# Kernel optimization log

Hardware: AMD Instinct MI355X
Metric: run time of the kernel (lower is better)

Reference implementation:

```python
import jax, jax.numpy as jnp
import numpy as np

N, IN_DIM, HID, OUT_DIM = 1024, 128, 128, 128


def setup_inputs() -> dict:
    key = jax.random.key(0)
    ks = jax.random.split(key, 7)
    s_in = 1.0 / np.sqrt(IN_DIM)
    s_h = 1.0 / np.sqrt(HID)
    return {
        "x": jax.random.normal(ks[0], (N, IN_DIM), jnp.float32),
        "W1": jax.random.normal(ks[1], (IN_DIM, HID), jnp.float32) * s_in,
        "b1": jax.random.normal(ks[2], (HID,), jnp.float32) * s_in,
        "W2": jax.random.normal(ks[3], (HID, 1), jnp.float32) * s_h,
        "b2": jax.random.normal(ks[4], (1,), jnp.float32) * s_h,
        "Wg": jax.random.normal(ks[5], (IN_DIM, OUT_DIM), jnp.float32) * s_in,
        "bg": jax.random.normal(ks[6], (OUT_DIM,), jnp.float32) * s_in,
    }


def reference(x, W1, b1, W2, b2, Wg, bg):
    # Pairwise abs-diff: [N, N, in_dim]
    diff = jnp.abs(x[:, None, :] - x[None, :, :])
    # 2-layer MLP -> scalar edge logit, then sigmoid -> dense adjacency [N, N]
    h = jax.nn.relu(jnp.einsum("ijd,dh->ijh", diff, W1) + b1)
    adj = jax.nn.sigmoid(jnp.einsum("ijh,ho->ijo", h, W2)[..., 0] + b2[0])
    # sigmoid > 0 everywhere => dense_to_sparse keeps ALL N^2 edges incl. diagonal;
    # PyG gcn_norm then adds no extra self-loops. Symmetric GCN normalization:
    deg = adj.sum(axis=1)  # adj is symmetric (|x_i - x_j| symmetric)
    dinv = jax.lax.rsqrt(deg)
    a_norm = dinv[:, None] * adj * dinv[None, :]
    out = a_norm @ (x @ Wg) + bg
    out = jnp.where(out > 0, out, 0.2 * out)  # leaky_relu(0.2)
    return out, adj
```

## Files before the change

kernel.cpp:

```cpp
#include <hip/hip_runtime.h>
#include <hip/hip_bf16.h>
#include <math.h>

typedef __attribute__((ext_vector_type(8))) _Float16 half8;
typedef __attribute__((ext_vector_type(2))) _Float16 half2v;
typedef __attribute__((ext_vector_type(4))) float f32x4;
typedef __attribute__((ext_vector_type(4))) unsigned int u32x4;

#define NPT 1024
#define D   128

__device__ __forceinline__ unsigned int absdiff_pk(unsigned int a, unsigned int b) {
  half2v d = __builtin_bit_cast(half2v, a) - __builtin_bit_cast(half2v, b);
  return __builtin_bit_cast(unsigned int, d) & 0x7FFF7FFFu;
}
__device__ __forceinline__ unsigned int pk_max(unsigned int a, unsigned int b) {
  unsigned int r;
  asm("v_pk_max_f16 %0, %1, %2" : "=v"(r) : "v"(a), "v"(b));
  return r;
}
__device__ __forceinline__ unsigned int pkrtz(float lo, float hi) {
  return __builtin_bit_cast(unsigned int, __builtin_amdgcn_cvt_pkrtz(lo, hi));
}
__device__ __forceinline__ float fdot2(unsigned int a, unsigned int b, float c) {
  return __builtin_amdgcn_fdot2(__builtin_bit_cast(half2v, a),
                                __builtin_bit_cast(half2v, b), c, false);
}

__global__ __launch_bounds__(128) void k_prep(const float* __restrict__ x,
                                              const float* __restrict__ W1,
                                              const float* __restrict__ Wg,
                                              unsigned short* __restrict__ xsw,
                                              unsigned short* __restrict__ w1p,
                                              unsigned short* __restrict__ xwghT) {
  __shared__ float xi[D];
  const int i = blockIdx.x;
  const int t = threadIdx.x;
  const float xv = x[i * D + t];
  xi[t] = xv;
  const _Float16 hv = (_Float16)xv;
  const int byte = i * 256 + ((2 * t) ^ ((i & 7) << 4));
  *(unsigned short*)((unsigned char*)xsw + byte) =
      __builtin_bit_cast(unsigned short, hv);
  if (i < 128) {
    const _Float16 wv = (_Float16)W1[t * 128 + i];
    w1p[((t >> 3) * 128 + i) * 8 + (t & 7)] = __builtin_bit_cast(unsigned short, wv);
  }
  __syncthreads();
  float a0 = 0.f, a1 = 0.f, a2 = 0.f, a3 = 0.f;
#pragma unroll 8
  for (int k = 0; k < D; k += 4) {
    a0 += xi[k + 0] * Wg[(k + 0) * D + t];
    a1 += xi[k + 1] * Wg[(k + 1) * D + t];
    a2 += xi[k + 2] * Wg[(k + 2) * D + t];
    a3 += xi[k + 3] * Wg[(k + 3) * D + t];
  }
  const _Float16 av = (_Float16)((a0 + a1) + (a2 + a3));
  xwghT[t * NPT + i] = __builtin_bit_cast(unsigned short, av);
}

__global__ __launch_bounds__(256, 2) void k_adj(const unsigned short* __restrict__ xsw,
                                                const unsigned short* __restrict__ w1p,
                                                const float* __restrict__ b1,
                                                const float* __restrict__ W2,
                                                const float* __restrict__ b2,
                                                float* __restrict__ adj) {
  __shared__ float sbuf[4][272];
  const int tid  = threadIdx.x;
  const int lane = tid & 63;
  const int w    = tid >> 6;
  const int l15  = lane & 15;
  const int g    = lane >> 4;
  const int i   = blockIdx.x * 4 + w;
  const int c   = blockIdx.y;
  const int i2  = 1023 - i;
  const int a   = i >> 4;
  const int n_i = 64 - a;
  const int ustart = c * 16;
  const int uend   = (c == 3) ? 65 : (ustart + 16);
  const int len    = uend - ustart;
  const int nvals  = len * 16;
  const int asc    = (blockIdx.x & 1) == 0;

  half8 w1f[4][8];
#pragma unroll
  for (int ks = 0; ks < 4; ++ks)
#pragma unroll
    for (int ht = 0; ht < 8; ++ht)
      w1f[ks][ht] = *(const half8*)(w1p + ((ks * 4 + g) * 128 + ht * 16 + l15) * 8);

  unsigned int nb1pk[8][2], w2pk[8][2];
  float c0 = 0.f;
#pragma unroll
  for (int ht = 0; ht < 8; ++ht) {
    const f32x4 bv = *(const f32x4*)&b1[ht * 16 + g * 4];
    const f32x4 wv = *(const f32x4*)&W2[ht * 16 + g * 4];
    c0 += bv[0] * wv[0] + bv[1] * wv[1] + bv[2] * wv[2] + bv[3] * wv[3];
    nb1pk[ht][0] = pkrtz(-bv[0], -bv[1]);
    nb1pk[ht][1] = pkrtz(-bv[2], -bv[3]);
    w2pk[ht][0] = pkrtz(wv[0], wv[1]);
    w2pk[ht][1] = pkrtz(wv[2], wv[3]);
  }
  c0 += __shfl_xor(c0, 16);
  c0 += __shfl_xor(c0, 32);
  const float B2 = b2[0] + c0;

  const unsigned char* xsb = (const unsigned char*)xsw;
  const unsigned char* jlane = xsb + l15 * 256;
  const int sxJ = (l15 & 7) << 4;
  const int kb0 = (0 * 64 + g * 16) ^ sxJ;
  const int kb1 = (1 * 64 + g * 16) ^ sxJ;
  const int kb2 = (2 * 64 + g * 16) ^ sxJ;
  const int kb3 = (3 * 64 + g * 16) ^ sxJ;

  float* sbw = sbuf[w];
  u32x4 xiu[4];
  int row_cur = -1;

  u32x4 jr0, jr1, jr2, jr3;
  {
    const int u0 = asc ? ustart : (uend - 1);
    const int grp0 = (u0 < n_i) ? (a + u0) : (u0 - 1);
    const unsigned char* cur = jlane + grp0 * 4096;
    jr0 = *(const u32x4*)(cur + kb0);
    jr1 = *(const u32x4*)(cur + kb1);
    jr2 = *(const u32x4*)(cur + kb2);
    jr3 = *(const u32x4*)(cur + kb3);
  }

#pragma unroll 1
  for (int t = 0; t < len; ++t) {
    const int u = asc ? (ustart + t) : (uend - 1 - t);
    const int row = (u < n_i) ? i : i2;
    if (row != row_cur) {
      row_cur = row;
      const unsigned char* xrow = xsb + row * 256;
      const int sxI = (row & 7) << 4;
#pragma unroll
      for (int ks = 0; ks < 4; ++ks)
        xiu[ks] = *(const u32x4*)(xrow + ((ks * 64 + g * 16) ^ sxI));
    }
    const int tn = (t + 1 < len) ? (t + 1) : t;
    const int un = asc ? (ustart + tn) : (uend - 1 - tn);
    const int grpn = (un < n_i) ? (a + un) : (un - 1);
    const unsigned char* nrow = jlane + grpn * 4096;

    f32x4 acc[8];
#pragma unroll
    for (int ht = 0; ht < 8; ++ht) acc[ht] = f32x4{0.f, 0.f, 0.f, 0.f};

    __builtin_amdgcn_s_setprio(1);
    {
      u32x4 afu;
#pragma unroll
      for (int p4 = 0; p4 < 4; ++p4) afu[p4] = absdiff_pk(jr0[p4], xiu[0][p4]);
      jr0 = *(const u32x4*)(nrow + kb0);
      const half8 af = __builtin_bit_cast(half8, afu);
#pragma unroll
      for (int ht = 0; ht < 8; ++ht)
        acc[ht] = __builtin_amdgcn_mfma_f32_16x16x32_f16(w1f[0][ht], af, acc[ht], 0, 0, 0);
    }
    {
      u32x4 afu;
#pragma unroll
      for (int p4 = 0; p4 < 4; ++p4) afu[p4] = absdiff_pk(jr1[p4], xiu[1][p4]);
      jr1 = *(const u32x4*)(nrow + kb1);
      const half8 af = __builtin_bit_cast(half8, afu);
#pragma unroll
      for (int ht = 0; ht < 8; ++ht)
        acc[ht] = __builtin_amdgcn_mfma_f32_16x16x32_f16(w1f[1][ht], af, acc[ht], 0, 0, 0);
    }
    {
      u32x4 afu;
#pragma unroll
      for (int p4 = 0; p4 < 4; ++p4) afu[p4] = absdiff_pk(jr2[p4], xiu[2][p4]);
      jr2 = *(const u32x4*)(nrow + kb2);
      const half8 af = __builtin_bit_cast(half8, afu);
#pragma unroll
      for (int ht = 0; ht < 8; ++ht)
        acc[ht] = __builtin_amdgcn_mfma_f32_16x16x32_f16(w1f[2][ht], af, acc[ht], 0, 0, 0);
    }
    {
      u32x4 afu;
#pragma unroll
      for (int p4 = 0; p4 < 4; ++p4) afu[p4] = absdiff_pk(jr3[p4], xiu[3][p4]);
      jr3 = *(const u32x4*)(nrow + kb3);
      const half8 af = __builtin_bit_cast(half8, afu);
#pragma unroll
      for (int ht = 0; ht < 8; ++ht)
        acc[ht] = __builtin_amdgcn_mfma_f32_16x16x32_f16(w1f[3][ht], af, acc[ht], 0, 0, 0);
    }
    __builtin_amdgcn_s_setprio(0);

    float sA = 0.f, sB = 0.f, sC = 0.f, sD = 0.f;
#pragma unroll
    for (int ht = 0; ht < 8; ht += 2) {
      unsigned int h0a = pk_max(pkrtz(acc[ht][0], acc[ht][1]), nb1pk[ht][0]);
      unsigned int h0b = pk_max(pkrtz(acc[ht][2], acc[ht][3]), nb1pk[ht][1]);
      unsigned int h1a = pk_max(pkrtz(acc[ht + 1][0], acc[ht + 1][1]), nb1pk[ht + 1][0]);
      unsigned int h1b = pk_max(pkrtz(acc[ht + 1][2], acc[ht + 1][3]), nb1pk[ht + 1][1]);
      sA = fdot2(h0a, w2pk[ht][0], sA);
      sB = fdot2(h0b, w2pk[ht][1], sB);
      sC = fdot2(h1a, w2pk[ht + 1][0], sC);
      sD = fdot2(h1b, w2pk[ht + 1][1], sD);
    }
    float s = (sA + sB) + (sC + sD);
    s += __shfl_xor(s, 16);
    s += __shfl_xor(s, 32);
    if (lane < 16) sbw[t * 16 + l15] = s;
  }

#pragma unroll 1
  for (int it = 0; it < 5; ++it) {
    const int p = it * 64 + lane;
    if (p < nvals) {
      const int tt = p >> 4;
      const int u = asc ? (ustart + tt) : (uend - 1 - tt);
      const int row = (u < n_i) ? i : i2;
      const int grp = (u < n_i) ? (a + u) : (u - 1);
      const float s = sbw[p];
      const float sig = 1.f / (1.f + __expf(-(s + B2)));
      adj[row * NPT + grp * 16 + (p & 15)] = sig;
    }
  }
}

__global__ __launch_bounds__(256) void k_sym(float* __restrict__ adj) {
  __shared__ float lds[4][16][17];
  const int tid  = threadIdx.x;
  const int lane = tid & 63;
  const int w    = tid >> 6;
  const int t = blockIdx.x * 4 + w;

  int R = (int)((1.0f + sqrtf(1.0f + 8.0f * (float)t)) * 0.5f);
  if (R * (R - 1) / 2 > t) --R;
  if ((R + 1) * R / 2 <= t) ++R;
  const int C = t - R * (R - 1) / 2;

  const int r16 = lane & 15;
  const int c4  = (lane >> 4) * 4;
  const f32x4 v = *(const f32x4*)&adj[(C * 16 + r16) * NPT + R * 16 + c4];
#pragma unroll
  for (int e = 0; e < 4; ++e) lds[w][c4 + e][r16] = v[e];
  f32x4 o;
#pragma unroll
  for (int e = 0; e < 4; ++e) o[e] = lds[w][r16][c4 + e];
  *(f32x4*)&adj[(R * 16 + r16) * NPT + C * 16 + c4] = o;
}

__global__ __launch_bounds__(256) void k_deg(const float* __restrict__ adj,
                                             float* __restrict__ deg) {
  const int lane = threadIdx.x & 63;
  const int w    = threadIdx.x >> 6;
  const int i = blockIdx.x * 4 + w;
  const float* row = &adj[i * NPT];
  float s = 0.f;
#pragma unroll
  for (int k = 0; k < 4; ++k) {
    const f32x4 v = *(const f32x4*)&row[(k * 64 + lane) * 4];
    s += (v[0] + v[1]) + (v[2] + v[3]);
  }
#pragma unroll
  for (int m = 1; m < 64; m <<= 1) s += __shfl_xor(s, m);
  if (lane == 0) deg[i] = s;
}

__global__ __launch_bounds__(128) void k_d1(const float* __restrict__ adj,
                                            const unsigned short* __restrict__ xwghT,
                                            const float* __restrict__ deg,
                                            const float* __restrict__ bg,
                                            float* __restrict__ outp) {
  __shared__ unsigned short dvh[NPT];
  const int tid  = threadIdx.x;
  const int lane = tid & 63;
  const int w    = tid >> 6;
  const int l15  = lane & 15;
  const int g    = lane >> 4;
  const int i0 = blockIdx.x * 16;
  const int t0 = (blockIdx.y * 2 + w) * 16;

#pragma unroll
  for (int it = 0; it < 8; ++it) {
    const int idx = it * 128 + tid;
    const _Float16 dh = (_Float16)rsqrtf(deg[idx]);
    dvh[idx] = __builtin_bit_cast(unsigned short, dh);
  }
  __syncthreads();

  f32x4 acc{0.f, 0.f, 0.f, 0.f};
#pragma unroll 2
  for (int ch = 0; ch < 32; ++ch) {
    const int kofs = ch * 32 + g * 8;
    const half8 af = *(const half8*)(xwghT + (t0 + l15) * NPT + kofs);
    const f32x4 av0 = *(const f32x4*)&adj[(i0 + l15) * NPT + kofs];
    const f32x4 av1 = *(const f32x4*)&adj[(i0 + l15) * NPT + kofs + 4];
    const half2v* dq = (const half2v*)(dvh + kofs);
    u32x4 bu;
    bu[0] = __builtin_bit_cast(unsigned int,
        half2v(__builtin_bit_cast(half2v, pkrtz(av0[0], av0[1])) * dq[0]));
    bu[1] = __builtin_bit_cast(unsigned int,
        half2v(__builtin_bit_cast(half2v, pkrtz(av0[2], av0[3])) * dq[1]));
    bu[2] = __builtin_bit_cast(unsigned int,
        half2v(__builtin_bit_cast(half2v, pkrtz(av1[0], av1[1])) * dq[2]));
    bu[3] = __builtin_bit_cast(unsigned int,
        half2v(__builtin_bit_cast(half2v, pkrtz(av1[2], av1[3])) * dq[3]));
    acc = __builtin_amdgcn_mfma_f32_16x16x32_f16(__builtin_bit_cast(half8, af),
                                                 __builtin_bit_cast(half8, bu), acc, 0, 0, 0);
  }
  const float di = rsqrtf(deg[i0 + l15]);
  const f32x4 bgv = *(const f32x4*)&bg[t0 + g * 4];
  f32x4 o;
#pragma unroll
  for (int r = 0; r < 4; ++r) {
    const float v = acc[r] * di + bgv[r];
    o[r] = v > 0.f ? v : 0.2f * v;
  }
  *(f32x4*)&outp[(i0 + l15) * D + t0 + g * 4] = o;
}

extern "C" void kernel_launch(void* const* d_in, const int* in_sizes, int n_in,
                              void* d_out, int out_size, void* d_ws, size_t ws_size,
                              hipStream_t stream) {
  const float* x  = (const float*)d_in[0];
  const float* W1 = (const float*)d_in[1];
  const float* b1 = (const float*)d_in[2];
  const float* W2 = (const float*)d_in[3];
  const float* b2 = (const float*)d_in[4];
  const float* Wg = (const float*)d_in[5];
  const float* bg = (const float*)d_in[6];

  float* outp = (float*)d_out;
  float* adj  = outp + NPT * D;
  unsigned char* ws = (unsigned char*)d_ws;
  float* deg            = (float*)ws;
  unsigned short* xsw   = (unsigned short*)(ws + 4096);
  unsigned short* w1p   = (unsigned short*)(ws + 4096 + 262144);
  unsigned short* xwghT = (unsigned short*)(ws + 4096 + 262144 + 32768);

  k_prep<<<NPT, 128, 0, stream>>>(x, W1, Wg, xsw, w1p, xwghT);
  k_adj<<<dim3(128, 4), 256, 0, stream>>>(xsw, w1p, b1, W2, b2, adj);
  k_sym<<<504, 256, 0, stream>>>(adj);
  k_deg<<<256, 256, 0, stream>>>(adj, deg);
  k_d1<<<dim3(64, 4), 128, 0, stream>>>(adj, xwghT, deg, bg, outp);
}
```

Measured before the change: 45.54 us.

## Fuse symmetrization and degree computation with atomics; defer cross-group reduction to LDS

Merges the transpose-mirror kernel and the row-degree kernel into one launch. Degrees are accumulated with atomicAdd from each 16x16 tile and its transpose, plus extra blocks for diagonal tiles, and deg is zeroed in the prep kernel. This removes a full re-read of the 4MB adjacency and one launch, at the cost of float atomics and non-deterministic summation order. In k_adj, the two cross-lane shuffles are replaced by writing all 64 partials to a larger LDS buffer and summing 4 entries at store time. The asc direction selector is also changed from blockIdx.x to blockIdx.y.

```diff
diff --git a/kernel.cpp b/kernel.cpp
--- a/kernel.cpp
+++ b/kernel.cpp
@@ -30,6 +30,7 @@
 __global__ __launch_bounds__(128) void k_prep(const float* __restrict__ x,
                                               const float* __restrict__ W1,
                                               const float* __restrict__ Wg,
+                                              float* __restrict__ deg,
                                               unsigned short* __restrict__ xsw,
                                               unsigned short* __restrict__ w1p,
                                               unsigned short* __restrict__ xwghT) {
@@ -38,6 +39,7 @@
   const int t = threadIdx.x;
   const float xv = x[i * D + t];
   xi[t] = xv;
+  if (t == 0) deg[i] = 0.f;
   const _Float16 hv = (_Float16)xv;
   const int byte = i * 256 + ((2 * t) ^ ((i & 7) << 4));
   *(unsigned short*)((unsigned char*)xsw + byte) =
@@ -65,7 +67,7 @@
                                                 const float* __restrict__ W2,
                                                 const float* __restrict__ b2,
                                                 float* __restrict__ adj) {
-  __shared__ float sbuf[4][272];
+  __shared__ float sbuf[4][17 * 68];
   const int tid  = threadIdx.x;
   const int lane = tid & 63;
   const int w    = tid >> 6;
@@ -80,7 +82,7 @@
   const int uend   = (c == 3) ? 65 : (ustart + 16);
   const int len    = uend - ustart;
   const int nvals  = len * 16;
-  const int asc    = (blockIdx.x & 1) == 0;
+  const int asc    = (blockIdx.y >> 1) & 1;
 
   half8 w1f[4][8];
 #pragma unroll
@@ -204,10 +206,7 @@
       sC = fdot2(h1a, w2pk[ht + 1][0], sC);
       sD = fdot2(h1b, w2pk[ht + 1][1], sD);
     }
-    float s = (sA + sB) + (sC + sD);
-    s += __shfl_xor(s, 16);
-    s += __shfl_xor(s, 32);
-    if (lane < 16) sbw[t * 16 + l15] = s;
+    sbw[t * 68 + lane] = (sA + sB) + (sC + sD);
   }
 
 #pragma unroll 1
@@ -215,54 +214,57 @@
     const int p = it * 64 + lane;
     if (p < nvals) {
       const int tt = p >> 4;
+      const int j = p & 15;
       const int u = asc ? (ustart + tt) : (uend - 1 - tt);
       const int row = (u < n_i) ? i : i2;
       const int grp = (u < n_i) ? (a + u) : (u - 1);
-      const float s = sbw[p];
+      const float s = sbw[tt * 68 + j] + sbw[tt * 68 + 16 + j] +
+                      sbw[tt * 68 + 32 + j] + sbw[tt * 68 + 48 + j];
       const float sig = 1.f / (1.f + __expf(-(s + B2)));
-      adj[row * NPT + grp * 16 + (p & 15)] = sig;
-    }
-  }
-}
-
-__global__ __launch_bounds__(256) void k_sym(float* __restrict__ adj) {
+      adj[row * NPT + grp * 16 + j] = sig;
+    }
+  }
+}
+
+__global__ __launch_bounds__(256) void k_symdeg(float* __restrict__ adj,
+                                                float* __restrict__ deg) {
   __shared__ float lds[4][16][17];
   const int tid  = threadIdx.x;
   const int lane = tid & 63;
   const int w    = tid >> 6;
-  const int t = blockIdx.x * 4 + w;
-
-  int R = (int)((1.0f + sqrtf(1.0f + 8.0f * (float)t)) * 0.5f);
-  if (R * (R - 1) / 2 > t) --R;
-  if ((R + 1) * R / 2 <= t) ++R;
-  const int C = t - R * (R - 1) / 2;
-
   const int r16 = lane & 15;
   const int c4  = (lane >> 4) * 4;
-  const f32x4 v = *(const f32x4*)&adj[(C * 16 + r16) * NPT + R * 16 + c4];
-#pragma unroll
-  for (int e = 0; e < 4; ++e) lds[w][c4 + e][r16] = v[e];
-  f32x4 o;
-#pragma unroll
-  for (int e = 0; e < 4; ++e) o[e] = lds[w][r16][c4 + e];
-  *(f32x4*)&adj[(R * 16 + r16) * NPT + C * 16 + c4] = o;
-}
-
-__global__ __launch_bounds__(256) void k_deg(const float* __restrict__ adj,
-                                             float* __restrict__ deg) {
-  const int lane = threadIdx.x & 63;
-  const int w    = threadIdx.x >> 6;
-  const int i = blockIdx.x * 4 + w;
-  const float* row = &adj[i * NPT];
-  float s = 0.f;
-#pragma unroll
-  for (int k = 0; k < 4; ++k) {
-    const f32x4 v = *(const f32x4*)&row[(k * 64 + lane) * 4];
-    s += (v[0] + v[1]) + (v[2] + v[3]);
-  }
-#pragma unroll
-  for (int m = 1; m < 64; m <<= 1) s += __shfl_xor(s, m);
-  if (lane == 0) deg[i] = s;
+
+  if (blockIdx.x < 504) {
+    const int t = blockIdx.x * 4 + w;
+    int R = (int)((1.0f + sqrtf(1.0f + 8.0f * (float)t)) * 0.5f);
+    if (R * (R - 1) / 2 > t) --R;
+    if ((R + 1) * R / 2 <= t) ++R;
+    const int C = t - R * (R - 1) / 2;
+
+    const f32x4 v = *(const f32x4*)&adj[(C * 16 + r16) * NPT + R * 16 + c4];
+    float rs = (v[0] + v[1]) + (v[2] + v[3]);
+    rs += __shfl_xor(rs, 16);
+    rs += __shfl_xor(rs, 32);
+    if (lane < 16) atomicAdd(&deg[C * 16 + r16], rs);
+#pragma unroll
+    for (int e = 0; e < 4; ++e) lds[w][c4 + e][r16] = v[e];
+    f32x4 o;
+#pragma unroll
+    for (int e = 0; e < 4; ++e) o[e] = lds[w][r16][c4 + e];
+    *(f32x4*)&adj[(R * 16 + r16) * NPT + C * 16 + c4] = o;
+    float cs = (o[0] + o[1]) + (o[2] + o[3]);
+    cs += __shfl_xor(cs, 16);
+    cs += __shfl_xor(cs, 32);
+    if (lane < 16) atomicAdd(&deg[R * 16 + r16], cs);
+  } else {
+    const int T = (blockIdx.x - 504) * 4 + w;
+    const f32x4 v = *(const f32x4*)&adj[(T * 16 + r16) * NPT + T * 16 + c4];
+    float rs = (v[0] + v[1]) + (v[2] + v[3]);
+    rs += __shfl_xor(rs, 16);
+    rs += __shfl_xor(rs, 32);
+    if (lane < 16) atomicAdd(&deg[T * 16 + r16], rs);
+  }
 }
 
 __global__ __launch_bounds__(128) void k_d1(const float* __restrict__ adj,
@@ -337,9 +339,8 @@
   unsigned short* w1p   = (unsigned short*)(ws + 4096 + 262144);
   unsigned short* xwghT = (unsigned short*)(ws + 4096 + 262144 + 32768);
 
-  k_prep<<<NPT, 128, 0, stream>>>(x, W1, Wg, xsw, w1p, xwghT);
+  k_prep<<<NPT, 128, 0, stream>>>(x, W1, Wg, deg, xsw, w1p, xwghT);
   k_adj<<<dim3(128, 4), 256, 0, stream>>>(xsw, w1p, b1, W2, b2, adj);
-  k_sym<<<504, 256, 0, stream>>>(adj);
-  k_deg<<<256, 256, 0, stream>>>(adj, deg);
+  k_symdeg<<<520, 256, 0, stream>>>(adj, deg);
   k_d1<<<dim3(64, 4), 128, 0, stream>>>(adj, xwghT, deg, bg, outp);
 }
```

Measured after the change: 44.08 us. 1.03x faster.
